# Performance work log

Measured on AMD Instinct MI355X. Metric: run time of the kernel, lower is better.

The kernel has to match this reference:

```python
import jax, jax.numpy as jnp
import numpy as np

N = 100000
E = 1600000
H = 128
M = 256
L = 6
G = 512          # number of graphs in the batch
A = 95           # num_atom_types
EXTRA = 3        # input_dim - 1
EPS = 1e-5


def swish(x):
    return x * jax.nn.sigmoid(x)


def setup_inputs() -> dict:
    key = jax.random.key(0)
    ks = jax.random.split(key, 16)
    z = jax.random.randint(ks[0], (N, 1), 0, A).astype(jnp.float32)
    extra = jax.random.normal(ks[1], (N, EXTRA), dtype=jnp.float32)
    x = jnp.concatenate([z, extra], axis=1)                     # [N, 4]
    edge_index = jax.random.randint(ks[2], (2, E), 0, N)        # [2, E]
    batch = jnp.sort(jax.random.randint(ks[3], (N,), 0, G))     # [N]
    s = 0.02
    z_embed = jax.random.normal(ks[4], (A, H), dtype=jnp.float32) * s
    extra_w = jax.random.normal(ks[5], (H, EXTRA), dtype=jnp.float32) * (1.0 / np.sqrt(EXTRA))
    extra_b = jnp.zeros((H,), jnp.float32)
    conv_w = jax.random.normal(ks[6], (L, H, H), dtype=jnp.float32) * (1.0 / np.sqrt(H))
    conv_b = jnp.zeros((L, H), jnp.float32)
    gamma = jnp.ones((L, H), jnp.float32)
    beta = jnp.zeros((L, H), jnp.float32)
    mean_scale = jnp.ones((L, H), jnp.float32)
    mlp_w1 = jax.random.normal(ks[7], (L, M, H), dtype=jnp.float32) * (1.0 / np.sqrt(H))
    mlp_b1 = jnp.zeros((L, M), jnp.float32)
    mlp_w2 = jax.random.normal(ks[8], (L, H, M), dtype=jnp.float32) * (1.0 / np.sqrt(M))
    mlp_b2 = jnp.zeros((L, H), jnp.float32)
    return dict(x=x, edge_index=edge_index, batch=batch, z_embed=z_embed,
                extra_w=extra_w, extra_b=extra_b, conv_w=conv_w, conv_b=conv_b,
                gamma=gamma, beta=beta, mean_scale=mean_scale,
                mlp_w1=mlp_w1, mlp_b1=mlp_b1, mlp_w2=mlp_w2, mlp_b2=mlp_b2)


def gnn_forward(x, edge_index, batch, z_embed, extra_w, extra_b, conv_w, conv_b,
                gamma, beta, mean_scale, mlp_w1, mlp_b1, mlp_w2, mlp_b2):
    z = x[:, 0].astype(jnp.int32)
    h = z_embed[z] + x[:, 1:] @ extra_w.T + extra_b                 # [N, H]

    # GCN: add self loops, symmetric normalization (computed once; graph is static)
    loop = jnp.arange(N)
    src = jnp.concatenate([edge_index[0], loop])
    dst = jnp.concatenate([edge_index[1], loop])
    deg = jax.ops.segment_sum(jnp.ones_like(dst, jnp.float32), dst, num_segments=N)
    dinv = jnp.where(deg > 0, jax.lax.rsqrt(jnp.maximum(deg, 1.0)), 0.0)
    norm = (dinv[src] * dinv[dst])[:, None]                         # [E+N, 1]

    cnt = jax.ops.segment_sum(jnp.ones((N,), jnp.float32), batch, num_segments=G)[:, None]
    cnt = jnp.maximum(cnt, 1.0)

    for i in range(L):
        h_res = h
        # GCNConv
        xw = h @ conv_w[i].T
        agg = jax.ops.segment_sum(xw[src] * norm, dst, num_segments=N) + conv_b[i]
        # GraphNorm: gamma * (x - alpha*mean) / sqrt(var + eps) + beta, per graph
        mean = jax.ops.segment_sum(agg, batch, num_segments=G) / cnt   # [G, H]
        sub = agg - mean_scale[i] * mean[batch]
        var = jax.ops.segment_sum(sub * sub, batch, num_segments=G) / cnt
        hn = gamma[i] * sub * jax.lax.rsqrt(var[batch] + EPS) + beta[i]
        ha = swish(hn)
        # residual MLP
        h = swish(swish(ha @ mlp_w1[i].T + mlp_b1[i]) @ mlp_w2[i].T + mlp_b2[i]) + h_res
    return h


def reference(x, edge_index, batch, z_embed, extra_w, extra_b, conv_w, conv_b,
              gamma, beta, mean_scale, mlp_w1, mlp_b1, mlp_w2, mlp_b2):
    return gnn_forward(x, edge_index, batch, z_embed, extra_w, extra_b, conv_w, conv_b,
                       gamma, beta, mean_scale, mlp_w1, mlp_b1, mlp_w2, mlp_b2)
```

## Files before the change

### kernel.cpp

```cpp
#include <hip/hip_runtime.h>

#define NN 100000
#define EE 1600000
#define HH 128
#define MM 256
#define LL 6
#define GG 512
#define SCAN_NB ((NN + 1023) / 1024)

typedef __attribute__((ext_vector_type(8))) short short8;
typedef __attribute__((ext_vector_type(4))) float floatx4;

__device__ __forceinline__ float swishf(float v) {
    return v / (1.0f + __expf(-v));
}

__device__ __forceinline__ unsigned short f2bf(float f) {
    unsigned u = __builtin_bit_cast(unsigned, f);
    unsigned r = u + 0x7FFFu + ((u >> 16) & 1u);
    return (unsigned short)(r >> 16);
}

__device__ __forceinline__ float bf2f(unsigned short u) {
    return __builtin_bit_cast(float, (unsigned)u << 16);
}

__device__ __forceinline__ float2 bf2f2(unsigned u) {
    float2 r;
    r.x = __builtin_bit_cast(float, u << 16);
    r.y = __builtin_bit_cast(float, u & 0xFFFF0000u);
    return r;
}

__device__ __forceinline__ void unpack8(uint4 v, float* a) {
    float2 p0 = bf2f2(v.x), p1 = bf2f2(v.y), p2 = bf2f2(v.z), p3 = bf2f2(v.w);
    a[0] = p0.x; a[1] = p0.y; a[2] = p1.x; a[3] = p1.y;
    a[4] = p2.x; a[5] = p2.y; a[6] = p3.x; a[7] = p3.y;
}

__device__ __forceinline__ uint4 pack8(const float* o) {
    uint4 pk;
    pk.x = (unsigned)f2bf(o[0]) | ((unsigned)f2bf(o[1]) << 16);
    pk.y = (unsigned)f2bf(o[2]) | ((unsigned)f2bf(o[3]) << 16);
    pk.z = (unsigned)f2bf(o[4]) | ((unsigned)f2bf(o[5]) << 16);
    pk.w = (unsigned)f2bf(o[6]) | ((unsigned)f2bf(o[7]) << 16);
    return pk;
}

__device__ __forceinline__ uint2 pack4(const float* o) {
    uint2 pk;
    pk.x = (unsigned)f2bf(o[0]) | ((unsigned)f2bf(o[1]) << 16);
    pk.y = (unsigned)f2bf(o[2]) | ((unsigned)f2bf(o[3]) << 16);
    return pk;
}

__global__ void k_embed(const float* __restrict__ x, const float* __restrict__ z_embed,
                        const float* __restrict__ ew, const float* __restrict__ eb,
                        unsigned short* __restrict__ hb) {
    int idx = blockIdx.x * blockDim.x + threadIdx.x;
    if (idx >= NN * 32) return;
    int n = idx >> 5;
    int c0 = (idx & 31) << 2;
    const float* xr = x + (size_t)n * 4;
    int z = (int)xr[0];
    float x1 = xr[1], x2 = xr[2], x3 = xr[3];
    const float* ze = z_embed + (size_t)z * HH + c0;
    float o[4];
#pragma unroll
    for (int j = 0; j < 4; ++j) {
        int c = c0 + j;
        o[j] = ze[j] + x1 * ew[c * 3 + 0] + x2 * ew[c * 3 + 1] + x3 * ew[c * 3 + 2] + eb[c];
    }
    *(uint2*)(hb + (size_t)n * HH + c0) = pack4(o);
}

__global__ void k_f2bf3(const float* __restrict__ s1, unsigned short* __restrict__ d1, int n1,
                        const float* __restrict__ s2, unsigned short* __restrict__ d2, int n2,
                        const float* __restrict__ s3, unsigned short* __restrict__ d3, int n3) {
    int i = blockIdx.x * blockDim.x + threadIdx.x;
    if (i < n1) {
        d1[i] = f2bf(s1[i]);
    } else if (i < n1 + n2) {
        d2[i - n1] = f2bf(s2[i - n1]);
    } else if (i < n1 + n2 + n3) {
        d3[i - n1 - n2] = f2bf(s3[i - n1 - n2]);
    }
}

__global__ __launch_bounds__(256) void k_degree_p(const int* __restrict__ dst,
                                                  int* __restrict__ deg) {
    int part = blockIdx.x & 7;
    int blk = blockIdx.x >> 3;
    int nb = gridDim.x >> 3;
    int lo = (int)((long long)part * NN / 8);
    int hi = (int)((long long)(part + 1) * NN / 8);
    for (int e = blk * 256 + threadIdx.x; e < EE; e += nb * 256) {
        int d = dst[e];
        if (d >= lo && d < hi) atomicAdd(&deg[d], 1);
    }
}

__global__ void k_dinv(const int* __restrict__ deg, float* __restrict__ dinv) {
    int n = blockIdx.x * blockDim.x + threadIdx.x;
    if (n < NN) dinv[n] = rsqrtf((float)(deg[n] + 1));
}

__global__ void k_scan1(const int* __restrict__ deg, int* __restrict__ bsum) {
    __shared__ int sd[256];
    int t = threadIdx.x;
    int base = blockIdx.x * 1024 + t * 4;
    int s = 0;
#pragma unroll
    for (int j = 0; j < 4; ++j) {
        int i = base + j;
        if (i < NN) s += deg[i];
    }
    sd[t] = s;
    __syncthreads();
    for (int off = 128; off > 0; off >>= 1) {
        if (t < off) sd[t] += sd[t + off];
        __syncthreads();
    }
    if (t == 0) bsum[blockIdx.x] = sd[0];
}

__global__ void k_scan2(const int* __restrict__ bsum, int* __restrict__ boff) {
    __shared__ int sd[128];
    int t = threadIdx.x;
    int v = (t < SCAN_NB) ? bsum[t] : 0;
    sd[t] = v;
    __syncthreads();
    for (int off = 1; off < 128; off <<= 1) {
        int u = (t >= off) ? sd[t - off] : 0;
        __syncthreads();
        sd[t] += u;
        __syncthreads();
    }
    boff[t] = sd[t] - v;
}

__global__ void k_scan3(const int* __restrict__ deg, const int* __restrict__ boff,
                        int* __restrict__ rowptr) {
    __shared__ int sd[256];
    int t = threadIdx.x;
    int base = blockIdx.x * 1024 + t * 4;
    int v[4];
    int s = 0;
#pragma unroll
    for (int j = 0; j < 4; ++j) {
        int i = base + j;
        v[j] = (i < NN) ? deg[i] : 0;
        s += v[j];
    }
    sd[t] = s;
    __syncthreads();
    for (int off = 1; off < 256; off <<= 1) {
        int u = (t >= off) ? sd[t - off] : 0;
        __syncthreads();
        sd[t] += u;
        __syncthreads();
    }
    int run = boff[blockIdx.x] + sd[t] - s;
#pragma unroll
    for (int j = 0; j < 4; ++j) {
        int i = base + j;
        if (i < NN) rowptr[i] = run;
        if (i == NN - 1) rowptr[NN] = run + v[j];
        run += v[j];
    }
}

__global__ __launch_bounds__(256) void k_fill_p(const int* __restrict__ ei,
                                                const int* __restrict__ rowptr,
                                                int* __restrict__ cursor,
                                                int* __restrict__ col) {
    int part = blockIdx.x & 7;
    int blk = blockIdx.x >> 3;
    int nb = gridDim.x >> 3;
    int lo = (int)((long long)part * NN / 8);
    int hi = (int)((long long)(part + 1) * NN / 8);
    for (int e = blk * 256 + threadIdx.x; e < EE; e += nb * 256) {
        int d = ei[EE + e];
        if (d >= lo && d < hi) {
            int p = atomicAdd(&cursor[d], 1);
            col[rowptr[d] + p] = ei[e];
        }
    }
}

__global__ void k_gptr(const int* __restrict__ batch, int* __restrict__ gptr) {
    int n = blockIdx.x * blockDim.x + threadIdx.x;
    if (n >= NN) return;
    int b = batch[n];
    int pb = (n == 0) ? -1 : batch[n - 1];
    for (int g = pb + 1; g <= b; ++g) gptr[g] = n;
    if (n == NN - 1) {
        for (int g = b + 1; g <= GG; ++g) gptr[g] = NN;
    }
}

__global__ __launch_bounds__(256) void k_conv(const unsigned short* __restrict__ A,
                                              const unsigned short* __restrict__ B,
                                              const float* __restrict__ dinv,
                                              unsigned short* __restrict__ Cb) {
    __shared__ unsigned short Bs[128][HH + 8];
    const int tid = threadIdx.x;
    const int wave = tid >> 6;
    const int lane = tid & 63;
    const int quad = lane >> 4;
    const int l16 = lane & 15;
    const int wr = (wave & 1) << 6;
    const int wc = (wave >> 1) << 6;
    const int rowBase = blockIdx.x * 128;

    for (int i = tid; i < 128 * (HH / 8); i += 256) {
        int r = i / (HH / 8);
        int kk = (i % (HH / 8)) * 8;
        int rho = (r & 64) | ((r & 3) << 4) | ((r >> 2) & 15);
        *(uint4*)(&Bs[rho][kk]) = *(const uint4*)(B + (size_t)r * HH + kk);
    }

    floatx4 acc[4][4];
    const floatx4 zed = {0.f, 0.f, 0.f, 0.f};
#pragma unroll
    for (int i = 0; i < 4; ++i)
#pragma unroll
        for (int j = 0; j < 4; ++j) acc[i][j] = zed;

    int ar[4];
#pragma unroll
    for (int i = 0; i < 4; ++i) {
        int r = rowBase + wr + (i << 4) + l16;
        ar[i] = r < NN ? r : NN - 1;
    }

    __syncthreads();

#pragma unroll
    for (int ks = 0; ks < HH / 32; ++ks) {
        int k = (ks << 5) + (quad << 3);
        short8 a[4], b[4];
#pragma unroll
        for (int i = 0; i < 4; ++i) a[i] = *(const short8*)(A + (size_t)ar[i] * HH + k);
#pragma unroll
        for (int j = 0; j < 4; ++j) b[j] = *(const short8*)(&Bs[wc + (j << 4) + l16][k]);
#pragma unroll
        for (int i = 0; i < 4; ++i)
#pragma unroll
            for (int j = 0; j < 4; ++j)
                acc[i][j] =
                    __builtin_amdgcn_mfma_f32_16x16x32_bf16(a[i], b[j], acc[i][j], 0, 0, 0);
    }

    const int c0 = wc + (l16 << 2);
#pragma unroll
    for (int i = 0; i < 4; ++i) {
        int rb = rowBase + wr + (i << 4) + (quad << 2);
#pragma unroll
        for (int reg = 0; reg < 4; ++reg) {
            int r = rb + reg;
            if (r < NN) {
                float dv = dinv[r];
                float o[4];
#pragma unroll
                for (int j = 0; j < 4; ++j) o[j] = acc[i][j][reg] * dv;
                *(uint2*)(Cb + (size_t)r * HH + c0) = pack4(o);
            }
        }
    }
}

__global__ __launch_bounds__(256) void k_agg(const unsigned short* __restrict__ y,
                                             const int* __restrict__ rowptr,
                                             const int* __restrict__ col,
                                             const float* __restrict__ dinv,
                                             const float* __restrict__ cb,
                                             const int* __restrict__ batch,
                                             unsigned short* __restrict__ agg,
                                             float* __restrict__ S1g,
                                             float* __restrict__ S2g) {
    __shared__ float s1s[4][128];
    __shared__ float s2s[4][128];
    __shared__ int sg[4];
    int w = threadIdx.x >> 6;
    int lane = threadIdx.x & 63;
    int d = blockIdx.x * 4 + w;
    bool valid = d < NN;
    int grp = lane >> 4;
    int l16 = lane & 15;
    const uint4* yv = (const uint4*)y;
    float acc[8];
#pragma unroll
    for (int j = 0; j < 8; ++j) acc[j] = 0.f;
    if (grp == 0 && valid) {
        uint4 v = yv[(size_t)d * 16 + l16];
        unpack8(v, acc);
    }
    int beg = 0, end = 0;
    if (valid) {
        beg = rowptr[d];
        end = rowptr[d + 1];
    }
    for (int e = beg + grp; e < end; e += 4) {
        int s = col[e];
        uint4 v = yv[(size_t)s * 16 + l16];
        float b0[8];
        unpack8(v, b0);
#pragma unroll
        for (int k = 0; k < 8; ++k) acc[k] += b0[k];
    }
#pragma unroll
    for (int j = 0; j < 8; ++j) {
        acc[j] += __shfl_xor(acc[j], 16, 64);
        acc[j] += __shfl_xor(acc[j], 32, 64);
    }
    if (grp == 0) {
        if (valid) {
            float dv = dinv[d];
            float4 c0 = *(const float4*)(cb + l16 * 8);
            float4 c1 = *(const float4*)(cb + l16 * 8 + 4);
            float o[8];
            o[0] = acc[0] * dv + c0.x; o[1] = acc[1] * dv + c0.y;
            o[2] = acc[2] * dv + c0.z; o[3] = acc[3] * dv + c0.w;
            o[4] = acc[4] * dv + c1.x; o[5] = acc[5] * dv + c1.y;
            o[6] = acc[6] * dv + c1.z; o[7] = acc[7] * dv + c1.w;
            unsigned short us[8];
#pragma unroll
            for (int j = 0; j < 8; ++j) us[j] = f2bf(o[j]);
            uint4 pk;
            pk.x = (unsigned)us[0] | ((unsigned)us[1] << 16);
            pk.y = (unsigned)us[2] | ((unsigned)us[3] << 16);
            pk.z = (unsigned)us[4] | ((unsigned)us[5] << 16);
            pk.w = (unsigned)us[6] | ((unsigned)us[7] << 16);
            *(uint4*)(agg + (size_t)d * HH + l16 * 8) = pk;
#pragma unroll
            for (int j = 0; j < 8; ++j) {
                float orv = bf2f(us[j]);
                s1s[w][l16 * 8 + j] = orv;
                s2s[w][l16 * 8 + j] = orv * orv;
            }
        } else {
#pragma unroll
            for (int j = 0; j < 8; ++j) {
                s1s[w][l16 * 8 + j] = 0.f;
                s2s[w][l16 * 8 + j] = 0.f;
            }
        }
        if (l16 == 0) sg[w] = valid ? batch[d] : -1;
    }
    __syncthreads();
    if (threadIdx.x < 128) {
        int c = threadIdx.x;
        int g0 = sg[0], g1 = sg[1], g2 = sg[2], g3 = sg[3];
        if (g0 >= 0 && g0 == g1 && g0 == g2 && g0 == g3) {
            float a = (s1s[0][c] + s1s[1][c]) + (s1s[2][c] + s1s[3][c]);
            float b = (s2s[0][c] + s2s[1][c]) + (s2s[2][c] + s2s[3][c]);
            atomicAdd(&S1g[g0 * HH + c], a);
            atomicAdd(&S2g[g0 * HH + c], b);
        } else {
            int gs[4] = {g0, g1, g2, g3};
#pragma unroll
            for (int ww = 0; ww < 4; ++ww) {
                if (gs[ww] >= 0) {
                    atomicAdd(&S1g[gs[ww] * HH + c], s1s[ww][c]);
                    atomicAdd(&S2g[gs[ww] * HH + c], s2s[ww][c]);
                }
            }
        }
    }
}

__global__ __launch_bounds__(128) void k_finalize(const int* __restrict__ gptr,
                                                  const float* __restrict__ ms,
                                                  const float* __restrict__ gamma,
                                                  const float* __restrict__ beta,
                                                  float* __restrict__ S1g,
                                                  float* __restrict__ S2g,
                                                  float* __restrict__ c1,
                                                  float* __restrict__ c0) {
    int g = blockIdx.x;
    int c = threadIdx.x;
    int cnt = gptr[g + 1] - gptr[g];
    float inv = 1.0f / (float)(cnt > 0 ? cnt : 1);
    float S1 = S1g[g * HH + c];
    float S2 = S2g[g * HH + c];
    float m = S1 * inv;
    float msc = ms[c];
    float var = S2 * inv - msc * (2.0f - msc) * m * m;
    float rstd = rsqrtf(var + 1e-5f);
    float c1v = gamma[c] * rstd;
    c1[g * HH + c] = c1v;
    c0[g * HH + c] = beta[c] - c1v * msc * m;
    S1g[g * HH + c] = 0.f;
    S2g[g * HH + c] = 0.f;
}

__global__ __launch_bounds__(256, 3) void k_mega(const unsigned short* __restrict__ agg,
                                                 const int* __restrict__ batch,
                                                 const float* __restrict__ c1,
                                                 const float* __restrict__ c0,
                                                 const unsigned short* __restrict__ W1,
                                                 const float* __restrict__ b1,
                                                 const unsigned short* __restrict__ W2,
                                                 const float* __restrict__ b2,
                                                 const unsigned short* __restrict__ Wc,
                                                 const float* __restrict__ dinv,
                                                 unsigned short* __restrict__ hb,
                                                 float* __restrict__ h_out,
                                                 unsigned short* __restrict__ y_out,
                                                 int writeF, int doConv) {
    __shared__ unsigned short ha_s[64 * 136];
    __shared__ unsigned short ts[64 * 264];
    const int tid = threadIdx.x;
    const int wave = tid >> 6;
    const int lane = tid & 63;
    const int quad = lane >> 4;
    const int l16 = lane & 15;
    const int rowBase = blockIdx.x * 64;
    const floatx4 zed = {0.f, 0.f, 0.f, 0.f};

    {
        int lr = tid >> 2;
        int coff = (tid & 3) << 5;
        int r = rowBase + lr;
        if (r >= NN) r = NN - 1;
        int g = batch[r];
        const float* c1p = c1 + g * HH + coff;
        const float* c0p = c0 + g * HH + coff;
#pragma unroll
        for (int q = 0; q < 4; ++q) {
            uint4 raw = *(const uint4*)(agg + (size_t)r * HH + coff + (q << 3));
            float v[8];
            unpack8(raw, v);
            float4 ca = *(const float4*)(c1p + (q << 3));
            float4 cb4 = *(const float4*)(c1p + (q << 3) + 4);
            float4 da = *(const float4*)(c0p + (q << 3));
            float4 db = *(const float4*)(c0p + (q << 3) + 4);
            float cc1[8] = {ca.x, ca.y, ca.z, ca.w, cb4.x, cb4.y, cb4.z, cb4.w};
            float cc0[8] = {da.x, da.y, da.z, da.w, db.x, db.y, db.z, db.w};
            float o[8];
#pragma unroll
            for (int j = 0; j < 8; ++j) o[j] = swishf(cc1[j] * v[j] + cc0[j]);
            *(uint4*)(&ha_s[lr * 136 + coff + (q << 3)]) = pack8(o);
        }
    }
    __syncthreads();

    {
        const int wca = wave << 6;
        floatx4 acc1[4][4];
#pragma unroll
        for (int i = 0; i < 4; ++i)
#pragma unroll
            for (int j = 0; j < 4; ++j) acc1[i][j] = zed;
#pragma unroll
        for (int ks = 0; ks < 4; ++ks) {
            int k = (ks << 5) + (quad << 3);
            short8 a[4], b[4];
#pragma unroll
            for (int i = 0; i < 4; ++i)
                a[i] = *(const short8*)(&ha_s[((i << 4) + l16) * 136 + k]);
#pragma unroll
            for (int j = 0; j < 4; ++j)
                b[j] = *(const short8*)(W1 + (size_t)(wca + (l16 << 2) + j) * HH + k);
#pragma unroll
            for (int i = 0; i < 4; ++i)
#pragma unroll
                for (int j = 0; j < 4; ++j)
                    acc1[i][j] =
                        __builtin_amdgcn_mfma_f32_16x16x32_bf16(a[i], b[j], acc1[i][j], 0, 0, 0);
        }
        const int ct = wca + (l16 << 2);
        float4 b4 = *(const float4*)(b1 + ct);
        float bv[4] = {b4.x, b4.y, b4.z, b4.w};
#pragma unroll
        for (int i = 0; i < 4; ++i) {
#pragma unroll
            for (int reg = 0; reg < 4; ++reg) {
                int lr = (i << 4) + (quad << 2) + reg;
                float o[4];
#pragma unroll
                for (int j = 0; j < 4; ++j) o[j] = swishf(acc1[i][j][reg] + bv[j]);
                *(uint2*)(&ts[lr * 264 + ct]) = pack4(o);
            }
        }
    }
    __syncthreads();

    const int wrb = (wave & 1) << 5;
    const int wcb = (wave >> 1) << 6;
    const int co = wcb + (l16 << 2);
    {
        floatx4 acc2[2][4];
#pragma unroll
        for (int i = 0; i < 2; ++i)
#pragma unroll
            for (int j = 0; j < 4; ++j) acc2[i][j] = zed;
#pragma unroll
        for (int ks = 0; ks < 8; ++ks) {
            int k = (ks << 5) + (quad << 3);
            short8 a[2], b[4];
#pragma unroll
            for (int i = 0; i < 2; ++i)
                a[i] = *(const short8*)(&ts[(wrb + (i << 4) + l16) * 264 + k]);
#pragma unroll
            for (int j = 0; j < 4; ++j)
                b[j] = *(const short8*)(W2 + (size_t)(wcb + (l16 << 2) + j) * MM + k);
#pragma unroll
            for (int i = 0; i < 2; ++i)
#pragma unroll
                for (int j = 0; j < 4; ++j)
                    acc2[i][j] =
                        __builtin_amdgcn_mfma_f32_16x16x32_bf16(a[i], b[j], acc2[i][j], 0, 0, 0);
        }
        float4 b4 = *(const float4*)(b2 + co);
        float bv[4] = {b4.x, b4.y, b4.z, b4.w};
#pragma unroll
        for (int i = 0; i < 2; ++i) {
#pragma unroll
            for (int reg = 0; reg < 4; ++reg) {
                int lr = wrb + (i << 4) + (quad << 2) + reg;
                int r = rowBase + lr;
                if (r < NN) {
                    uint2 rv = *(const uint2*)(hb + (size_t)r * HH + co);
                    float2 r01 = bf2f2(rv.x), r23 = bf2f2(rv.y);
                    float o[4];
                    o[0] = swishf(acc2[i][0][reg] + bv[0]) + r01.x;
                    o[1] = swishf(acc2[i][1][reg] + bv[1]) + r01.y;
                    o[2] = swishf(acc2[i][2][reg] + bv[2]) + r23.x;
                    o[3] = swishf(acc2[i][3][reg] + bv[3]) + r23.y;
                    uint2 pk = pack4(o);
                    *(uint2*)(hb + (size_t)r * HH + co) = pk;
                    if (writeF)
                        *(float4*)(h_out + (size_t)r * HH + co) =
                            make_float4(o[0], o[1], o[2], o[3]);
                    *(uint2*)(&ha_s[lr * 136 + co]) = pk;
                } else {
                    *(uint2*)(&ha_s[lr * 136 + co]) = make_uint2(0u, 0u);
                }
            }
        }
    }

    if (doConv) {
        __syncthreads();
        floatx4 acc3[2][4];
#pragma unroll
        for (int i = 0; i < 2; ++i)
#pragma unroll
            for (int j = 0; j < 4; ++j) acc3[i][j] = zed;
#pragma unroll
        for (int ks = 0; ks < 4; ++ks) {
            int k = (ks << 5) + (quad << 3);
            short8 a[2], b[4];
#pragma unroll
            for (int i = 0; i < 2; ++i)
                a[i] = *(const short8*)(&ha_s[(wrb + (i << 4) + l16) * 136 + k]);
#pragma unroll
            for (int j = 0; j < 4; ++j)
                b[j] = *(const short8*)(Wc + (size_t)(wcb + (l16 << 2) + j) * HH + k);
#pragma unroll
            for (int i = 0; i < 2; ++i)
#pragma unroll
                for (int j = 0; j < 4; ++j)
                    acc3[i][j] =
                        __builtin_amdgcn_mfma_f32_16x16x32_bf16(a[i], b[j], acc3[i][j], 0, 0, 0);
        }
#pragma unroll
        for (int i = 0; i < 2; ++i) {
#pragma unroll
            for (int reg = 0; reg < 4; ++reg) {
                int r = rowBase + wrb + (i << 4) + (quad << 2) + reg;
                if (r < NN) {
                    float dv = dinv[r];
                    float o[4];
#pragma unroll
                    for (int j = 0; j < 4; ++j) o[j] = acc3[i][j][reg] * dv;
                    *(uint2*)(y_out + (size_t)r * HH + co) = pack4(o);
                }
            }
        }
    }
}

extern "C" void kernel_launch(void* const* d_in, const int* in_sizes, int n_in,
                              void* d_out, int out_size, void* d_ws, size_t ws_size,
                              hipStream_t stream) {
    const float* x = (const float*)d_in[0];
    const int* ei = (const int*)d_in[1];
    const int* batch = (const int*)d_in[2];
    const float* z_embed = (const float*)d_in[3];
    const float* extra_w = (const float*)d_in[4];
    const float* extra_b = (const float*)d_in[5];
    const float* conv_w = (const float*)d_in[6];
    const float* conv_b = (const float*)d_in[7];
    const float* gamma = (const float*)d_in[8];
    const float* beta = (const float*)d_in[9];
    const float* mean_scale = (const float*)d_in[10];
    const float* mlp_w1 = (const float*)d_in[11];
    const float* mlp_b1 = (const float*)d_in[12];
    const float* mlp_w2 = (const float*)d_in[13];
    const float* mlp_b2 = (const float*)d_in[14];
    float* h_out = (float*)d_out;

    char* wsB = (char*)d_ws;
    size_t off = 0;
    auto alloc = [&](size_t bytes) -> void* {
        void* p = (void*)(wsB + off);
        off = (off + bytes + 255) & ~(size_t)255;
        return p;
    };
    float* dinv = (float*)alloc((size_t)NN * 4);
    int* deg = (int*)alloc((size_t)NN * 4);
    int* cursor = (int*)alloc((size_t)NN * 4);
    int* rowptr = (int*)alloc((size_t)(NN + 1) * 4);
    int* bsum = (int*)alloc(128 * 4);
    int* boff = (int*)alloc(128 * 4);
    int* col = (int*)alloc((size_t)EE * 4);
    int* gptr = (int*)alloc((size_t)(GG + 1) * 4);
    float* c1t = (float*)alloc((size_t)GG * HH * 4);
    float* c0t = (float*)alloc((size_t)GG * HH * 4);
    float* S1g = (float*)alloc((size_t)GG * HH * 4);
    float* S2g = (float*)alloc((size_t)GG * HH * 4);
    unsigned short* wb =
        (unsigned short*)alloc((size_t)(LL * (HH * HH + MM * HH + HH * MM)) * 2);
    unsigned short* cwb = wb;
    unsigned short* w1b = wb + (size_t)LL * HH * HH;
    unsigned short* w2b = w1b + (size_t)LL * MM * HH;
    unsigned short* hb = (unsigned short*)alloc((size_t)NN * HH * 2);
    unsigned short* ybuf = (unsigned short*)alloc((size_t)NN * HH * 2);
    unsigned short* aggb = (unsigned short*)alloc((size_t)NN * HH * 2);

    hipMemsetAsync(deg, 0, (size_t)NN * 4, stream);
    hipMemsetAsync(cursor, 0, (size_t)NN * 4, stream);
    hipMemsetAsync(S1g, 0, (size_t)GG * HH * 4, stream);
    hipMemsetAsync(S2g, 0, (size_t)GG * HH * 4, stream);

    k_embed<<<(NN * 32 + 255) / 256, 256, 0, stream>>>(x, z_embed, extra_w, extra_b, hb);
    {
        int n1 = LL * HH * HH, n2 = LL * MM * HH, n3 = LL * HH * MM;
        int nt = n1 + n2 + n3;
        k_f2bf3<<<(nt + 255) / 256, 256, 0, stream>>>(conv_w, cwb, n1, mlp_w1, w1b, n2,
                                                      mlp_w2, w2b, n3);
    }
    k_degree_p<<<1024, 256, 0, stream>>>(ei + EE, deg);
    k_dinv<<<(NN + 255) / 256, 256, 0, stream>>>(deg, dinv);
    k_scan1<<<SCAN_NB, 256, 0, stream>>>(deg, bsum);
    k_scan2<<<1, 128, 0, stream>>>(bsum, boff);
    k_scan3<<<SCAN_NB, 256, 0, stream>>>(deg, boff, rowptr);
    k_fill_p<<<1024, 256, 0, stream>>>(ei, rowptr, cursor, col);
    k_gptr<<<(NN + 255) / 256, 256, 0, stream>>>(batch, gptr);

    int gconv = (NN + 127) / 128;
    int gmega = (NN + 63) / 64;
    k_conv<<<gconv, 256, 0, stream>>>(hb, cwb, dinv, ybuf);
    for (int i = 0; i < LL; ++i) {
        k_agg<<<(NN + 3) / 4, 256, 0, stream>>>(ybuf, rowptr, col, dinv,
                                                conv_b + (size_t)i * HH, batch, aggb, S1g,
                                                S2g);
        k_finalize<<<GG, 128, 0, stream>>>(gptr, mean_scale + (size_t)i * HH,
                                           gamma + (size_t)i * HH, beta + (size_t)i * HH,
                                           S1g, S2g, c1t, c0t);
        k_mega<<<gmega, 256, 0, stream>>>(
            aggb, batch, c1t, c0t, w1b + (size_t)i * MM * HH, mlp_b1 + (size_t)i * MM,
            w2b + (size_t)i * HH * MM, mlp_b2 + (size_t)i * HH,
            cwb + (size_t)(i + 1 < LL ? i + 1 : 0) * HH * HH, dinv, hb, h_out, ybuf,
            i == LL - 1 ? 1 : 0, i < LL - 1 ? 1 : 0);
    }
}
```

Before: 1.332 ms.

## Split MLP hidden dim into halves to shrink LDS and raise occupancy; use packed bf16 convert

The fused MLP kernel now computes the 256-wide hidden layer in two 128-column halves, feeding each half straight into the second GEMM. This halves the hidden-activation shared-memory buffer and the first-GEMM accumulator registers, so the launch bound can rise from 3 to 4 blocks per CU. It also replaces the manual float-to-bf16 rounding with the hardware packed convert instruction in all pack helpers and in the aggregation kernel. The cost is extra barriers per block, and the convert may round differently at edge cases.

```diff
diff --git a/kernel.cpp b/kernel.cpp
--- a/kernel.cpp
+++ b/kernel.cpp
@@ -32,6 +32,12 @@
     return r;
 }
 
+__device__ __forceinline__ unsigned cvt2bf(float a, float b) {
+    unsigned r;
+    asm("v_cvt_pk_bf16_f32 %0, %1, %2" : "=v"(r) : "v"(a), "v"(b));
+    return r;
+}
+
 __device__ __forceinline__ void unpack8(uint4 v, float* a) {
     float2 p0 = bf2f2(v.x), p1 = bf2f2(v.y), p2 = bf2f2(v.z), p3 = bf2f2(v.w);
     a[0] = p0.x; a[1] = p0.y; a[2] = p1.x; a[3] = p1.y;
@@ -40,17 +46,17 @@
 
 __device__ __forceinline__ uint4 pack8(const float* o) {
     uint4 pk;
-    pk.x = (unsigned)f2bf(o[0]) | ((unsigned)f2bf(o[1]) << 16);
-    pk.y = (unsigned)f2bf(o[2]) | ((unsigned)f2bf(o[3]) << 16);
-    pk.z = (unsigned)f2bf(o[4]) | ((unsigned)f2bf(o[5]) << 16);
-    pk.w = (unsigned)f2bf(o[6]) | ((unsigned)f2bf(o[7]) << 16);
+    pk.x = cvt2bf(o[0], o[1]);
+    pk.y = cvt2bf(o[2], o[3]);
+    pk.z = cvt2bf(o[4], o[5]);
+    pk.w = cvt2bf(o[6], o[7]);
     return pk;
 }
 
 __device__ __forceinline__ uint2 pack4(const float* o) {
     uint2 pk;
-    pk.x = (unsigned)f2bf(o[0]) | ((unsigned)f2bf(o[1]) << 16);
-    pk.y = (unsigned)f2bf(o[2]) | ((unsigned)f2bf(o[3]) << 16);
+    pk.x = cvt2bf(o[0], o[1]);
+    pk.y = cvt2bf(o[2], o[3]);
     return pk;
 }
 
@@ -324,20 +330,14 @@
             o[2] = acc[2] * dv + c0.z; o[3] = acc[3] * dv + c0.w;
             o[4] = acc[4] * dv + c1.x; o[5] = acc[5] * dv + c1.y;
             o[6] = acc[6] * dv + c1.z; o[7] = acc[7] * dv + c1.w;
-            unsigned short us[8];
-#pragma unroll
-            for (int j = 0; j < 8; ++j) us[j] = f2bf(o[j]);
-            uint4 pk;
-            pk.x = (unsigned)us[0] | ((unsigned)us[1] << 16);
-            pk.y = (unsigned)us[2] | ((unsigned)us[3] << 16);
-            pk.z = (unsigned)us[4] | ((unsigned)us[5] << 16);
-            pk.w = (unsigned)us[6] | ((unsigned)us[7] << 16);
+            uint4 pk = pack8(o);
             *(uint4*)(agg + (size_t)d * HH + l16 * 8) = pk;
+            float2 q0 = bf2f2(pk.x), q1 = bf2f2(pk.y), q2 = bf2f2(pk.z), q3 = bf2f2(pk.w);
+            float orv[8] = {q0.x, q0.y, q1.x, q1.y, q2.x, q2.y, q3.x, q3.y};
 #pragma unroll
             for (int j = 0; j < 8; ++j) {
-                float orv = bf2f(us[j]);
-                s1s[w][l16 * 8 + j] = orv;
-                s2s[w][l16 * 8 + j] = orv * orv;
+                s1s[w][l16 * 8 + j] = orv[j];
+                s2s[w][l16 * 8 + j] = orv[j] * orv[j];
             }
         } else {
 #pragma unroll
@@ -395,7 +395,7 @@
     S2g[g * HH + c] = 0.f;
 }
 
-__global__ __launch_bounds__(256, 3) void k_mega(const unsigned short* __restrict__ agg,
+__global__ __launch_bounds__(256, 4) void k_mega(const unsigned short* __restrict__ agg,
                                                  const int* __restrict__ batch,
                                                  const float* __restrict__ c1,
                                                  const float* __restrict__ c0,
@@ -410,7 +410,7 @@
                                                  unsigned short* __restrict__ y_out,
                                                  int writeF, int doConv) {
     __shared__ unsigned short ha_s[64 * 136];
-    __shared__ unsigned short ts[64 * 264];
+    __shared__ unsigned short ts[64 * 136];
     const int tid = threadIdx.x;
     const int wave = tid >> 6;
     const int lane = tid & 63;
@@ -446,47 +446,6 @@
     }
     __syncthreads();
 
-    {
-        const int wca = wave << 6;
-        floatx4 acc1[4][4];
-#pragma unroll
-        for (int i = 0; i < 4; ++i)
-#pragma unroll
-            for (int j = 0; j < 4; ++j) acc1[i][j] = zed;
-#pragma unroll
-        for (int ks = 0; ks < 4; ++ks) {
-            int k = (ks << 5) + (quad << 3);
-            short8 a[4], b[4];
-#pragma unroll
-            for (int i = 0; i < 4; ++i)
-                a[i] = *(const short8*)(&ha_s[((i << 4) + l16) * 136 + k]);
-#pragma unroll
-            for (int j = 0; j < 4; ++j)
-                b[j] = *(const short8*)(W1 + (size_t)(wca + (l16 << 2) + j) * HH + k);
-#pragma unroll
-            for (int i = 0; i < 4; ++i)
-#pragma unroll
-                for (int j = 0; j < 4; ++j)
-                    acc1[i][j] =
-                        __builtin_amdgcn_mfma_f32_16x16x32_bf16(a[i], b[j], acc1[i][j], 0, 0, 0);
-        }
-        const int ct = wca + (l16 << 2);
-        float4 b4 = *(const float4*)(b1 + ct);
-        float bv[4] = {b4.x, b4.y, b4.z, b4.w};
-#pragma unroll
-        for (int i = 0; i < 4; ++i) {
-#pragma unroll
-            for (int reg = 0; reg < 4; ++reg) {
-                int lr = (i << 4) + (quad << 2) + reg;
-                float o[4];
-#pragma unroll
-                for (int j = 0; j < 4; ++j) o[j] = swishf(acc1[i][j][reg] + bv[j]);
-                *(uint2*)(&ts[lr * 264 + ct]) = pack4(o);
-            }
-        }
-    }
-    __syncthreads();
-
     const int wrb = (wave & 1) << 5;
     const int wcb = (wave >> 1) << 6;
     const int co = wcb + (l16 << 2);
@@ -496,23 +455,66 @@
         for (int i = 0; i < 2; ++i)
 #pragma unroll
             for (int j = 0; j < 4; ++j) acc2[i][j] = zed;
-#pragma unroll
-        for (int ks = 0; ks < 8; ++ks) {
-            int k = (ks << 5) + (quad << 3);
-            short8 a[2], b[4];
-#pragma unroll
-            for (int i = 0; i < 2; ++i)
-                a[i] = *(const short8*)(&ts[(wrb + (i << 4) + l16) * 264 + k]);
-#pragma unroll
-            for (int j = 0; j < 4; ++j)
-                b[j] = *(const short8*)(W2 + (size_t)(wcb + (l16 << 2) + j) * MM + k);
-#pragma unroll
-            for (int i = 0; i < 2; ++i)
+
+#pragma unroll
+        for (int h = 0; h < 2; ++h) {
+            floatx4 acc1[4][2];
+#pragma unroll
+            for (int i = 0; i < 4; ++i)
+#pragma unroll
+                for (int j = 0; j < 2; ++j) acc1[i][j] = zed;
+            const int tcol = (wave << 5) + (l16 << 1);
+#pragma unroll
+            for (int ks = 0; ks < 4; ++ks) {
+                int k = (ks << 5) + (quad << 3);
+                short8 a[4], b[2];
+#pragma unroll
+                for (int i = 0; i < 4; ++i)
+                    a[i] = *(const short8*)(&ha_s[((i << 4) + l16) * 136 + k]);
+#pragma unroll
+                for (int j = 0; j < 2; ++j)
+                    b[j] = *(const short8*)(W1 + (size_t)((h << 7) + tcol + j) * HH + k);
+#pragma unroll
+                for (int i = 0; i < 4; ++i)
+#pragma unroll
+                    for (int j = 0; j < 2; ++j)
+                        acc1[i][j] = __builtin_amdgcn_mfma_f32_16x16x32_bf16(a[i], b[j],
+                                                                             acc1[i][j], 0, 0, 0);
+            }
+            float2 bv = *(const float2*)(b1 + (h << 7) + tcol);
+#pragma unroll
+            for (int i = 0; i < 4; ++i) {
+#pragma unroll
+                for (int reg = 0; reg < 4; ++reg) {
+                    int lr = (i << 4) + (quad << 2) + reg;
+                    float o0 = swishf(acc1[i][0][reg] + bv.x);
+                    float o1 = swishf(acc1[i][1][reg] + bv.y);
+                    *(unsigned*)(&ts[lr * 136 + tcol]) = cvt2bf(o0, o1);
+                }
+            }
+            __syncthreads();
+
+#pragma unroll
+            for (int ks = 0; ks < 4; ++ks) {
+                int k = (ks << 5) + (quad << 3);
+                short8 a[2], b[4];
+#pragma unroll
+                for (int i = 0; i < 2; ++i)
+                    a[i] = *(const short8*)(&ts[(wrb + (i << 4) + l16) * 136 + k]);
 #pragma unroll
                 for (int j = 0; j < 4; ++j)
-                    acc2[i][j] =
-                        __builtin_amdgcn_mfma_f32_16x16x32_bf16(a[i], b[j], acc2[i][j], 0, 0, 0);
-        }
+                    b[j] = *(const short8*)(W2 + (size_t)(wcb + (l16 << 2) + j) * MM +
+                                            (h << 7) + k);
+#pragma unroll
+                for (int i = 0; i < 2; ++i)
+#pragma unroll
+                    for (int j = 0; j < 4; ++j)
+                        acc2[i][j] = __builtin_amdgcn_mfma_f32_16x16x32_bf16(a[i], b[j],
+                                                                             acc2[i][j], 0, 0, 0);
+            }
+            if (h == 0) __syncthreads();
+        }
+
         float4 b4 = *(const float4*)(b2 + co);
         float bv[4] = {b4.x, b4.y, b4.z, b4.w};
 #pragma unroll
```

New measurement: 1.283 ms. -3.7%, faster.
